# Kernel tuning notes

Measured on AMD Instinct MI355X. Metric: run time of the kernel, lower is better.

Reference implementation:

```python
import jax, jax.numpy as jnp
import numpy as np

N = 50000          # nodes
E = 800000         # edges
F_IN = 128         # in_channels
C = 64             # cell channels
NCELLS = 2
STEPS = 4
MULT = 4
N_EDGE_SLOTS = 14  # 2+3+4+5 mixed-op edges per cell
N_OPS = 8          # switch_on
NUM_CLASSES = 40
BN_EPS = 1e-5
GCNII_ALPHA = 0.1


def setup_inputs() -> dict:
    key = jax.random.key(0)
    ks = jax.random.split(key, 20)
    def w(k, shape, fan_in):
        return jax.random.normal(k, shape, dtype=jnp.float32) / np.float32(np.sqrt(fan_in))
    return {
        "x": jax.random.normal(ks[0], (N, F_IN), dtype=jnp.float32),
        "edge_index": jax.random.randint(ks[1], (2, E), 0, N, dtype=jnp.int32),
        "alphas": 0.001 * jax.random.normal(ks[2], (N_EDGE_SLOTS, N_OPS), dtype=jnp.float32),
        "stem_W": w(ks[3], (F_IN, 3 * C), F_IN),
        "pre_W": w(ks[4], (F_IN, C), F_IN),
        "pre0_W0": w(ks[5], (3 * C, C), 3 * C),
        "pre1_W0": w(ks[6], (3 * C, C), 3 * C),
        "pre0_W1": w(ks[7], (3 * C, C), 3 * C),
        "pre1_W1": w(ks[8], (MULT * C, C), MULT * C),
        "W_gcn": w(ks[9], (NCELLS, N_EDGE_SLOTS, C, C), C),
        "W_sage_self": w(ks[10], (NCELLS, N_EDGE_SLOTS, C, C), C),
        "W_sage_nei": w(ks[11], (NCELLS, N_EDGE_SLOTS, C, C), C),
        "W_gin": w(ks[12], (NCELLS, N_EDGE_SLOTS, C, C), C),
        "W_gc1": w(ks[13], (NCELLS, N_EDGE_SLOTS, C, C), C),
        "W_gc2": w(ks[14], (NCELLS, N_EDGE_SLOTS, C, C), C),
        "W_mlp": w(ks[15], (NCELLS, N_EDGE_SLOTS, C, C), C),
        "W_gcnii": w(ks[16], (NCELLS, N_EDGE_SLOTS, C, C), C),
        "cls_W": w(ks[17], (MULT * C + 1, NUM_CLASSES), MULT * C + 1),
        "cls_b": jnp.zeros((NUM_CLASSES,), dtype=jnp.float32),
    }


def reference(x, edge_index, alphas, stem_W, pre_W, pre0_W0, pre1_W0, pre0_W1, pre1_W1,
              W_gcn, W_sage_self, W_sage_nei, W_gin, W_gc1, W_gc2, W_mlp, W_gcnii,
              cls_W, cls_b):
    src, dst = edge_index[0], edge_index[1]
    deg = jax.ops.segment_sum(jnp.ones((E,), jnp.float32), dst, num_segments=N)
    deg = jnp.maximum(deg, 1.0)
    inv_deg = 1.0 / deg
    inv_sqrt = jax.lax.rsqrt(deg)
    edge_norm = (inv_sqrt[src] * inv_sqrt[dst])[:, None]  # [E,1] sym-normalized coeff

    def bn(h):  # batch norm over node axis, no affine (gamma=1, beta=0)
        m = jnp.mean(h, axis=0)
        v = jnp.var(h, axis=0)
        return (h - m) * jax.lax.rsqrt(v + BN_EPS)

    def mlp(xx, W, act):  # Linear(no bias) -> BN -> optional ReLU
        h = bn(xx @ W)
        return jnp.maximum(h, 0.0) if act else h

    relu = lambda t: jnp.maximum(t, 0.0)

    def mixed_op(h, wv, ci, ej, x0):
        # shared message-passing aggregations of h over edge_index
        msg = h[src]                                             # [E,C] gather
        s_sum = jax.ops.segment_sum(msg, dst, num_segments=N)    # sum agg
        s_mean = s_sum * inv_deg[:, None]                        # mean agg
        s_norm = jax.ops.segment_sum(msg * edge_norm, dst, num_segments=N)  # gcn agg
        out = wv[1] * h                                          # skip_connect (wv[0]: none)
        out = out + wv[2] * relu(s_norm @ W_gcn[ci, ej])
        out = out + wv[3] * (h @ W_sage_self[ci, ej] + s_mean @ W_sage_nei[ci, ej])
        out = out + wv[4] * relu((h + s_sum) @ W_gin[ci, ej])
        out = out + wv[5] * (h @ W_gc1[ci, ej] + s_sum @ W_gc2[ci, ej])
        out = out + wv[6] * relu(h @ W_mlp[ci, ej])
        out = out + wv[7] * relu(((1.0 - GCNII_ALPHA) * s_norm + GCNII_ALPHA * x0) @ W_gcnii[ci, ej])
        return out

    wmix = jax.nn.softmax(alphas, axis=-1)  # [14,8], identical across cells

    s0 = s1 = mlp(x, stem_W, act=False)     # stem: MLP([in, 3C], act=None)
    x0 = mlp(x, pre_W, act=True)            # preprocess: MLP([in, C], relu)
    pre_ws = [(pre0_W0, pre1_W0), (pre0_W1, pre1_W1)]
    for ci in range(NCELLS):
        p0, p1 = pre_ws[ci]
        a = mlp(s0, p0, act=True)
        b = mlp(s1, p1, act=True)
        states = [a, b]
        offset = 0
        for _ in range(STEPS):
            s = None
            for j, h in enumerate(states):
                o = mixed_op(h, wmix[offset + j], ci, offset + j, x0)
                s = o if s is None else s + o
            offset += len(states)
            states.append(s)
        out_cell = jnp.concatenate(states[-MULT:], axis=1)  # [N, 4C]
        s0, s1 = s1, out_cell

    pooled = jnp.mean(s1, axis=1, keepdims=True)            # AdaptiveAvgPool1d(1) over channels
    logits = jnp.concatenate([pooled, s1], axis=1) @ cls_W + cls_b
    return logits
```

## Files before the change

kernel.cpp:

```cpp
#include <hip/hip_runtime.h>
#include <stdint.h>

typedef unsigned short u16;
typedef __attribute__((ext_vector_type(8))) short bh8;
typedef __attribute__((ext_vector_type(4))) float f4;

__device__ __forceinline__ float b2f(u16 u){ union{unsigned u; float f;} x; x.u = ((unsigned)u)<<16; return x.f; }
__device__ __forceinline__ u16 f2b(float f){ union{float f; unsigned u;} x; x.f = f; return (u16)((x.u + 0x7fffu + ((x.u>>16)&1u))>>16); }
__device__ __forceinline__ bh8 ld8(const u16* p){ return *reinterpret_cast<const bh8*>(p); }

__device__ __forceinline__ int xcd_swz(int bid, int nwg){
  int q = nwg >> 3, r = nwg & 7;
  int x = bid & 7, k = bid >> 3;
  return (x < r ? x*(q+1) : r*(q+1) + (x - r)*q) + k;
}

#define NBK 512

__global__ __launch_bounds__(256) void k_hist(const int* dst, int* hist, int E){
  __shared__ int h[NBK];
  for (int i=threadIdx.x;i<NBK;i+=256) h[i]=0;
  __syncthreads();
  int stride = 256*gridDim.x;
  for (int i = blockIdx.x*256+threadIdx.x; i<E; i+=stride)
    atomicAdd(&h[dst[i]>>7], 1);
  __syncthreads();
  for (int i=threadIdx.x;i<NBK;i+=256){
    int v=h[i]; if (v) atomicAdd(&hist[i], v);
  }
}

__global__ __launch_bounds__(512) void k_scanb(const int* hist, int* bbase, int* bcursor){
  int t = threadIdx.x, lane = t&63, wv = t>>6;
  __shared__ int ws[8];
  int v = hist[t];
  int x = v;
  #pragma unroll
  for (int o=1;o<64;o<<=1){ int u=__shfl_up(x,(unsigned)o,64); if(lane>=o) x+=u; }
  if (lane==63) ws[wv]=x;
  __syncthreads();
  if (t<8){
    int s=ws[t];
    #pragma unroll
    for (int o=1;o<8;o<<=1){ int u=__shfl_up(s,(unsigned)o,8); if (t>=o) s+=u; }
    ws[t]=s;
  }
  __syncthreads();
  int base = (wv==0)?0:ws[wv-1];
  int ex = base + x - v;
  bbase[t]=ex; bcursor[t]=ex;
  if (t==511) bbase[512]=ex+v;
}

__global__ __launch_bounds__(256) void k_bucket(const int* src, const int* dst,
                                                int* bcursor, unsigned* bkt, int E, int nblk){
  __shared__ int h[NBK], base[NBK], lc[NBK];
  int per = (E + nblk - 1)/nblk;
  int e0 = blockIdx.x*per, e1 = min(E, e0+per);
  for (int i=threadIdx.x;i<NBK;i+=256){ h[i]=0; lc[i]=0; }
  __syncthreads();
  for (int e=e0+threadIdx.x; e<e1; e+=256) atomicAdd(&h[dst[e]>>7], 1);
  __syncthreads();
  for (int i=threadIdx.x;i<NBK;i+=256){
    int c=h[i]; base[i] = c ? atomicAdd(&bcursor[i], c) : 0;
  }
  __syncthreads();
  for (int e=e0+threadIdx.x; e<e1; e+=256){
    int d = dst[e];
    int b = d>>7;
    int r = atomicAdd(&lc[b], 1);
    bkt[base[b]+r] = ((unsigned)(d&127)<<25) | (unsigned)src[e];
  }
}

__global__ __launch_bounds__(128) void k_degb(const unsigned* bkt, const int* bbase,
                                              int* off, float* inv_deg, float* invs,
                                              int N, int E){
  int b = blockIdx.x, t = threadIdx.x;
  __shared__ int cnt[128];
  __shared__ int w0tot;
  cnt[t]=0;
  __syncthreads();
  int e0=bbase[b], e1=bbase[b+1];
  for (int e=e0+t; e<e1; e+=128) atomicAdd(&cnt[bkt[e]>>25], 1);
  __syncthreads();
  int v = cnt[t];
  int lane=t&63, wv=t>>6;
  int x=v;
  #pragma unroll
  for (int o=1;o<64;o<<=1){ int u=__shfl_up(x,(unsigned)o,64); if(lane>=o) x+=u; }
  if (t==63) w0tot=x;
  __syncthreads();
  int ex = x - v + (wv ? w0tot : 0);
  int node = b*128 + t;
  if (node < N){
    off[node] = e0 + ex;
    int d = (v<1)?1:v;
    float df=(float)d;
    inv_deg[node]=1.0f/df;
    invs[node]=rsqrtf(df);
  }
  if (b==0 && t==0) off[N]=E;
}

__global__ __launch_bounds__(128) void k_fillb(const unsigned* bkt, const int* bbase,
                                               const int* off, const float* invs,
                                               int2* csr, int N){
  int b = blockIdx.x, t = threadIdx.x;
  __shared__ int cur[128];
  int node = b*128 + t;
  cur[t] = (node < N) ? off[node] : 0;
  __syncthreads();
  int e0=bbase[b], e1=bbase[b+1];
  for (int e=e0+t; e<e1; e+=128){
    unsigned v = bkt[e];
    int i = (int)(v>>25);
    int s = (int)(v & 0x1FFFFFFu);
    int pos = atomicAdd(&cur[i], 1);
    csr[pos] = make_int2(s, __float_as_int(invs[s]));
  }
}

__global__ void k_softmax(const float* alphas, float* wmix){
  int t = threadIdx.x; int r = t >> 3, o = t & 7;
  if (r < 14){
    float v = alphas[r*8+o];
    float m = v;
    #pragma unroll
    for (int d=1; d<8; d<<=1) m = fmaxf(m, __shfl_xor(m, d, 8));
    float e = expf(v - m);
    float s = e;
    #pragma unroll
    for (int d=1; d<8; d<<=1) s += __shfl_xor(s, d, 8);
    wmix[r*8+o] = e / s;
  }
}

__global__ void k_f2b(const float* a, u16* b, int n){
  int i = blockIdx.x*256 + threadIdx.x;
  if (i < n) b[i] = f2b(a[i]);
}

struct PackAllArgs {
  const float* src[7];
  u16* dst[7];
  int K[7], ncol[7];
  int base[8];
};
__global__ __launch_bounds__(256) void k_packall(PackAllArgs P){
  int i = blockIdx.x*256 + threadIdx.x;
  if (i >= P.base[7]) return;
  int s = 0;
  #pragma unroll
  for (int k=1;k<7;k++) if (i >= P.base[k]) s = k;
  int e = i - P.base[s];
  if (s < 6){
    int K = P.K[s], ncol = P.ncol[s];
    int k = e / ncol, n = e - k*ncol;
    P.dst[s][(size_t)n*K + k] = f2b(P.src[s][e]);
  } else {
    int n = e >> 8, k = e & 255;
    float v = 0.f;
    if (n < 40) v = P.src[6][(size_t)(1+k)*40 + n] + P.src[6][n] * (1.f/256.f);
    P.dst[6][(size_t)n*256 + k] = f2b(v);
  }
}

struct PackArgs { const float* W[8]; const float* wmix; u16* dst; };
__global__ void k_pack_ops8(PackArgs P){
  int i = blockIdx.x*256 + threadIdx.x;
  if (i >= 28*8*4096) return;
  int slot28 = i >> 15;
  int rem = i & 32767;
  int mat = rem >> 12;
  int e = rem & 4095;
  int k = e >> 6, n = e & 63;
  const float* wm = P.wmix + (slot28 % 14)*8;
  size_t off = (size_t)slot28*4096 + e;
  float v = 0.f;
  switch(mat){
    case 0: v = wm[2]*P.W[0][off]; break;
    case 1: v = wm[3]*P.W[1][off] + wm[5]*P.W[4][off] + ((k==n) ? wm[1] : 0.f); break;
    case 2: v = wm[3]*P.W[2][off]; break;
    case 3: v = wm[4]*P.W[3][off]; break;
    case 4: v = wm[5]*P.W[5][off]; break;
    case 5: v = wm[6]*P.W[6][off]; break;
    case 6: v = 0.9f*wm[7]*P.W[7][off]; break;
    case 7: v = 0.1f*wm[7]*P.W[7][off]; break;
  }
  P.dst[(((size_t)slot28*8 + mat)<<12) + (n<<6) + (((k>>3) ^ (n&7))<<3) + (k&7)] = f2b(v);
}

template<int NT, int NKB>
__global__ __launch_bounds__(256) void k_gemm(const u16* A, const u16* Bp,
                                              u16* Tb, int Nn, float* Sp){
  const int K = NKB*32;
  const int ldT = NT*16;
  __shared__ float sred[4][NT*16][2];
  int tid = threadIdx.x, wv = tid>>6, lane = tid&63, q = lane>>4, t = lane&15;
  int row0 = blockIdx.x*128 + wv*32;
  f4 acc[2][NT];
  #pragma unroll
  for (int a=0;a<2;a++)
    #pragma unroll
    for (int b=0;b<NT;b++) acc[a][b] = (f4){0.f,0.f,0.f,0.f};
  const u16* arow0 = A + (size_t)(row0 + t)*K + q*8;
  const u16* arow1 = arow0 + (size_t)16*K;
  const u16* brow  = Bp + (size_t)t*K + q*8;
  #pragma unroll
  for (int kb = 0; kb < NKB; ++kb){
    bh8 a0 = ld8(arow0 + kb*32);
    bh8 a1 = ld8(arow1 + kb*32);
    #pragma unroll
    for (int nt=0; nt<NT; ++nt){
      bh8 bf = ld8(brow + (size_t)nt*16*K + kb*32);
      acc[0][nt] = __builtin_amdgcn_mfma_f32_16x16x32_bf16(a0, bf, acc[0][nt], 0, 0, 0);
      acc[1][nt] = __builtin_amdgcn_mfma_f32_16x16x32_bf16(a1, bf, acc[1][nt], 0, 0, 0);
    }
  }
  #pragma unroll
  for (int nt=0;nt<NT;nt++){
    float ps = 0.f, pq = 0.f;
    #pragma unroll
    for (int rt=0;rt<2;rt++)
      #pragma unroll
      for (int r=0;r<4;r++){
        int row = row0 + rt*16 + q*4 + r;
        float v = acc[rt][nt][r];
        if (row < Nn){
          Tb[(size_t)row*ldT + nt*16 + t] = f2b(v);
          ps += v; pq += v*v;
        }
      }
    ps += __shfl_xor(ps, 16, 64); pq += __shfl_xor(pq, 16, 64);
    ps += __shfl_xor(ps, 32, 64); pq += __shfl_xor(pq, 32, 64);
    if (q == 0){ sred[wv][nt*16 + t][0] = ps; sred[wv][nt*16 + t][1] = pq; }
  }
  __syncthreads();
  if (tid < NT*16){
    float s = sred[0][tid][0] + sred[1][tid][0] + sred[2][tid][0] + sred[3][tid][0];
    float qq = sred[0][tid][1] + sred[1][tid][1] + sred[2][tid][1] + sred[3][tid][1];
    float* sp = Sp + (size_t)blockIdx.x*(2*NT*16);
    sp[tid] = s;
    sp[NT*16 + tid] = qq;
  }
}

__global__ __launch_bounds__(256) void k_redstats(const float* Sp, float* S, int ncol, int nb){
  int c2 = blockIdx.x*4 + (threadIdx.x>>6);
  int lane = threadIdx.x & 63;
  if (c2 >= 2*ncol) return;
  int stride = 2*ncol;
  float s = 0.f;
  for (int b = lane; b < nb; b += 64) s += Sp[(size_t)b*stride + c2];
  #pragma unroll
  for (int m=1; m<64; m<<=1) s += __shfl_xor(s, m, 64);
  if (lane == 0){
    int c = (c2 < ncol) ? c2 : (256 + (c2 - ncol));
    S[c] = s;
  }
}

__global__ void k_norm(const u16* Tb, int ldT, int ncols, int Nn, const float* S,
                       u16* out, int rs_out, int relu, float invN){
  int i = blockIdx.x*256 + threadIdx.x;
  int nv = ncols >> 3;
  if (i >= Nn*nv) return;
  int r = i / nv, c8 = (i - r*nv)*8;
  bh8 tv = ld8(Tb + (size_t)r*ldT + c8);
  bh8 ov;
  #pragma unroll
  for (int u=0; u<8; ++u){
    int c = c8 + u;
    float m = S[c]*invN;
    float var = S[256+c]*invN - m*m;
    float xv = (b2f((u16)tv[u]) - m) * rsqrtf(var + 1e-5f);
    if (relu) xv = fmaxf(xv, 0.f);
    ov[u] = (short)f2b(xv);
  }
  *reinterpret_cast<bh8*>(out + (size_t)r*rs_out + c8) = ov;
}

__global__ void k_norm2(const u16* Tb, int Nn, const float* S,
                        u16* o1, u16* o2, float invN){
  int i = blockIdx.x*256 + threadIdx.x;
  if (i >= Nn*32) return;
  int r = i >> 5, c8 = (i & 31) << 3;
  bh8 tv = ld8(Tb + (size_t)r*256 + c8);
  bh8 ov;
  int relu = (c8 >= 192);
  #pragma unroll
  for (int u=0; u<8; ++u){
    int c = c8 + u;
    float m = S[c]*invN;
    float var = S[256+c]*invN - m*m;
    float xv = (b2f((u16)tv[u]) - m) * rsqrtf(var + 1e-5f);
    if (relu) xv = fmaxf(xv, 0.f);
    ov[u] = (short)f2b(xv);
  }
  if (c8 < 192)
    *reinterpret_cast<bh8*>(o1 + (size_t)r*192 + c8) = ov;
  else
    *reinterpret_cast<bh8*>(o2 + (size_t)r*64 + (c8 - 192)) = ov;
}

#define ACC8(vv, ww) { \
    float c0=__uint_as_float((vv).x<<16), c1=__uint_as_float((vv).x&0xffff0000u); \
    float c2=__uint_as_float((vv).y<<16), c3=__uint_as_float((vv).y&0xffff0000u); \
    float c4=__uint_as_float((vv).z<<16), c5=__uint_as_float((vv).z&0xffff0000u); \
    float c6=__uint_as_float((vv).w<<16), c7=__uint_as_float((vv).w&0xffff0000u); \
    s0+=c0; s1+=c1; s2+=c2; s3+=c3; s4+=c4; s5+=c5; s6+=c6; s7+=c7; \
    n0+=c0*(ww); n1+=c1*(ww); n2+=c2*(ww); n3+=c3*(ww); \
    n4+=c4*(ww); n5+=c5*(ww); n6+=c6*(ww); n7+=c7*(ww); }

template<int SHIFT>
__global__ __launch_bounds__(256) void k_aggv(const u16* h, const int* off, const int2* csr,
                                              const float* inv_sqrt, u16* out_sum, u16* out_norm, int Nn){
  int blk = xcd_swz(blockIdx.x, gridDim.x);
  int g = blk*8 + (threadIdx.x >> 5);
  if (g >= Nn) return;
  int l32 = threadIdx.x & 31;
  int sub = l32 >> 3;
  int cb = (l32 & 7) << 3;
  const u16* hp = h + cb;
  float s0=0,s1=0,s2=0,s3=0,s4=0,s5=0,s6=0,s7=0;
  float n0=0,n1=0,n2=0,n3=0,n4=0,n5=0,n6=0,n7=0;
  int e0 = off[g], e1 = off[g+1];
  int e = e0 + sub;
  for (; e + 12 < e1; e += 16){
    int2 cA = csr[e];
    int2 cB = csr[e+4];
    int2 cC = csr[e+8];
    int2 cD = csr[e+12];
    uint4 vA = *reinterpret_cast<const uint4*>(hp + (((unsigned)cA.x) << SHIFT));
    uint4 vB = *reinterpret_cast<const uint4*>(hp + (((unsigned)cB.x) << SHIFT));
    uint4 vC = *reinterpret_cast<const uint4*>(hp + (((unsigned)cC.x) << SHIFT));
    uint4 vD = *reinterpret_cast<const uint4*>(hp + (((unsigned)cD.x) << SHIFT));
    float wA = __int_as_float(cA.y), wB = __int_as_float(cB.y);
    float wC = __int_as_float(cC.y), wD = __int_as_float(cD.y);
    ACC8(vA, wA)
    ACC8(vB, wB)
    ACC8(vC, wC)
    ACC8(vD, wD)
  }
  for (; e < e1; e += 4){
    int2 cA = csr[e];
    uint4 vA = *reinterpret_cast<const uint4*>(hp + (((unsigned)cA.x) << SHIFT));
    float wA = __int_as_float(cA.y);
    ACC8(vA, wA)
  }
  #pragma unroll
  for (int m = 8; m <= 16; m <<= 1){
    s0 += __shfl_xor(s0,m,64); s1 += __shfl_xor(s1,m,64);
    s2 += __shfl_xor(s2,m,64); s3 += __shfl_xor(s3,m,64);
    s4 += __shfl_xor(s4,m,64); s5 += __shfl_xor(s5,m,64);
    s6 += __shfl_xor(s6,m,64); s7 += __shfl_xor(s7,m,64);
    n0 += __shfl_xor(n0,m,64); n1 += __shfl_xor(n1,m,64);
    n2 += __shfl_xor(n2,m,64); n3 += __shfl_xor(n3,m,64);
    n4 += __shfl_xor(n4,m,64); n5 += __shfl_xor(n5,m,64);
    n6 += __shfl_xor(n6,m,64); n7 += __shfl_xor(n7,m,64);
  }
  if (sub == 0){
    float ig = inv_sqrt[g];
    uint4 o;
    o.x = (uint)f2b(s0) | ((uint)f2b(s1) << 16);
    o.y = (uint)f2b(s2) | ((uint)f2b(s3) << 16);
    o.z = (uint)f2b(s4) | ((uint)f2b(s5) << 16);
    o.w = (uint)f2b(s6) | ((uint)f2b(s7) << 16);
    *reinterpret_cast<uint4*>(out_sum + (size_t)g*64 + cb) = o;
    o.x = (uint)f2b(n0*ig) | ((uint)f2b(n1*ig) << 16);
    o.y = (uint)f2b(n2*ig) | ((uint)f2b(n3*ig) << 16);
    o.z = (uint)f2b(n4*ig) | ((uint)f2b(n5*ig) << 16);
    o.w = (uint)f2b(n6*ig) | ((uint)f2b(n7*ig) << 16);
    *reinterpret_cast<uint4*>(out_norm + (size_t)g*64 + cb) = o;
  }
}

#define ACC8AB(va, vb, ww) { \
    float a0=__uint_as_float((va).x<<16), a1=__uint_as_float((va).x&0xffff0000u); \
    float a2=__uint_as_float((va).y<<16), a3=__uint_as_float((va).y&0xffff0000u); \
    float a4=__uint_as_float((va).z<<16), a5=__uint_as_float((va).z&0xffff0000u); \
    float a6=__uint_as_float((va).w<<16), a7=__uint_as_float((va).w&0xffff0000u); \
    float b0=__uint_as_float((vb).x<<16), b1=__uint_as_float((vb).x&0xffff0000u); \
    float b2=__uint_as_float((vb).y<<16), b3=__uint_as_float((vb).y&0xffff0000u); \
    float b4=__uint_as_float((vb).z<<16), b5=__uint_as_float((vb).z&0xffff0000u); \
    float b6=__uint_as_float((vb).w<<16), b7=__uint_as_float((vb).w&0xffff0000u); \
    sa0+=a0; sa1+=a1; sa2+=a2; sa3+=a3; sa4+=a4; sa5+=a5; sa6+=a6; sa7+=a7; \
    na0+=a0*(ww); na1+=a1*(ww); na2+=a2*(ww); na3+=a3*(ww); \
    na4+=a4*(ww); na5+=a5*(ww); na6+=a6*(ww); na7+=a7*(ww); \
    sb0+=b0; sb1+=b1; sb2+=b2; sb3+=b3; sb4+=b4; sb5+=b5; sb6+=b6; sb7+=b7; \
    nb0+=b0*(ww); nb1+=b1*(ww); nb2+=b2*(ww); nb3+=b3*(ww); \
    nb4+=b4*(ww); nb5+=b5*(ww); nb6+=b6*(ww); nb7+=b7*(ww); }

__global__ __launch_bounds__(256) void k_agg2v(const u16* ab, const int* off, const int2* csr,
                                               const float* inv_sqrt,
                                               u16* os0, u16* on0, u16* os1, u16* on1, int Nn){
  int blk = xcd_swz(blockIdx.x, gridDim.x);
  int g = blk*8 + (threadIdx.x >> 5);
  if (g >= Nn) return;
  int l32 = threadIdx.x & 31;
  int sub = l32 >> 3;
  int cb = (l32 & 7) << 3;
  const u16* hp = ab + cb;
  float sa0=0,sa1=0,sa2=0,sa3=0,sa4=0,sa5=0,sa6=0,sa7=0;
  float na0=0,na1=0,na2=0,na3=0,na4=0,na5=0,na6=0,na7=0;
  float sb0=0,sb1=0,sb2=0,sb3=0,sb4=0,sb5=0,sb6=0,sb7=0;
  float nb0=0,nb1=0,nb2=0,nb3=0,nb4=0,nb5=0,nb6=0,nb7=0;
  int e0 = off[g], e1 = off[g+1];
  int e = e0 + sub;
  for (; e + 4 < e1; e += 8){
    int2 cA = csr[e];
    int2 cB = csr[e+4];
    const u16* rpA = hp + (((unsigned)cA.x) << 7);
    const u16* rpB = hp + (((unsigned)cB.x) << 7);
    uint4 vaA = *reinterpret_cast<const uint4*>(rpA);
    uint4 vbA = *reinterpret_cast<const uint4*>(rpA + 64);
    uint4 vaB = *reinterpret_cast<const uint4*>(rpB);
    uint4 vbB = *reinterpret_cast<const uint4*>(rpB + 64);
    float wA = __int_as_float(cA.y), wB = __int_as_float(cB.y);
    ACC8AB(vaA, vbA, wA)
    ACC8AB(vaB, vbB, wB)
  }
  if (e < e1){
    int2 cA = csr[e];
    const u16* rpA = hp + (((unsigned)cA.x) << 7);
    uint4 vaA = *reinterpret_cast<const uint4*>(rpA);
    uint4 vbA = *reinterpret_cast<const uint4*>(rpA + 64);
    float wA = __int_as_float(cA.y);
    ACC8AB(vaA, vbA, wA)
  }
  #pragma unroll
  for (int m = 8; m <= 16; m <<= 1){
    sa0 += __shfl_xor(sa0,m,64); sa1 += __shfl_xor(sa1,m,64);
    sa2 += __shfl_xor(sa2,m,64); sa3 += __shfl_xor(sa3,m,64);
    sa4 += __shfl_xor(sa4,m,64); sa5 += __shfl_xor(sa5,m,64);
    sa6 += __shfl_xor(sa6,m,64); sa7 += __shfl_xor(sa7,m,64);
    na0 += __shfl_xor(na0,m,64); na1 += __shfl_xor(na1,m,64);
    na2 += __shfl_xor(na2,m,64); na3 += __shfl_xor(na3,m,64);
    na4 += __shfl_xor(na4,m,64); na5 += __shfl_xor(na5,m,64);
    na6 += __shfl_xor(na6,m,64); na7 += __shfl_xor(na7,m,64);
    sb0 += __shfl_xor(sb0,m,64); sb1 += __shfl_xor(sb1,m,64);
    sb2 += __shfl_xor(sb2,m,64); sb3 += __shfl_xor(sb3,m,64);
    sb4 += __shfl_xor(sb4,m,64); sb5 += __shfl_xor(sb5,m,64);
    sb6 += __shfl_xor(sb6,m,64); sb7 += __shfl_xor(sb7,m,64);
    nb0 += __shfl_xor(nb0,m,64); nb1 += __shfl_xor(nb1,m,64);
    nb2 += __shfl_xor(nb2,m,64); nb3 += __shfl_xor(nb3,m,64);
    nb4 += __shfl_xor(nb4,m,64); nb5 += __shfl_xor(nb5,m,64);
    nb6 += __shfl_xor(nb6,m,64); nb7 += __shfl_xor(nb7,m,64);
  }
  if (sub == 0){
    float ig = inv_sqrt[g];
    uint4 o;
    o.x = (uint)f2b(sa0) | ((uint)f2b(sa1) << 16);
    o.y = (uint)f2b(sa2) | ((uint)f2b(sa3) << 16);
    o.z = (uint)f2b(sa4) | ((uint)f2b(sa5) << 16);
    o.w = (uint)f2b(sa6) | ((uint)f2b(sa7) << 16);
    *reinterpret_cast<uint4*>(os0 + (size_t)g*64 + cb) = o;
    o.x = (uint)f2b(na0*ig) | ((uint)f2b(na1*ig) << 16);
    o.y = (uint)f2b(na2*ig) | ((uint)f2b(na3*ig) << 16);
    o.z = (uint)f2b(na4*ig) | ((uint)f2b(na5*ig) << 16);
    o.w = (uint)f2b(na6*ig) | ((uint)f2b(na7*ig) << 16);
    *reinterpret_cast<uint4*>(on0 + (size_t)g*64 + cb) = o;
    o.x = (uint)f2b(sb0) | ((uint)f2b(sb1) << 16);
    o.y = (uint)f2b(sb2) | ((uint)f2b(sb3) << 16);
    o.z = (uint)f2b(sb4) | ((uint)f2b(sb5) << 16);
    o.w = (uint)f2b(sb6) | ((uint)f2b(sb7) << 16);
    *reinterpret_cast<uint4*>(os1 + (size_t)g*64 + cb) = o;
    o.x = (uint)f2b(nb0*ig) | ((uint)f2b(nb1*ig) << 16);
    o.y = (uint)f2b(nb2*ig) | ((uint)f2b(nb3*ig) << 16);
    o.z = (uint)f2b(nb4*ig) | ((uint)f2b(nb5*ig) << 16);
    o.w = (uint)f2b(nb6*ig) | ((uint)f2b(nb7*ig) << 16);
    *reinterpret_cast<uint4*>(on1 + (size_t)g*64 + cb) = o;
  }
}

struct StepArgs {
  const u16* h[5]; const u16* asum[5]; const u16* anorm[5];
  int rs[5]; int slot[5]; int J;
  const u16* wpk; const float* inv_deg; const u16* x0;
  u16* out; int rs_out; int Nn;
};

__device__ __forceinline__ void mm8(const bh8 (&af)[2], const u16* wlds, int mat,
                                    int t, int q, f4 (&acc)[4]){
  #pragma unroll
  for (int kb=0;kb<2;kb++)
    #pragma unroll
    for (int nt=0;nt<4;nt++){
      bh8 bf = ld8(wlds + (mat<<12) + ((nt*16+t)<<6) + ((((kb<<2)|q) ^ (t&7))<<3));
      acc[nt] = __builtin_amdgcn_mfma_f32_16x16x32_bf16(af[kb], bf, acc[nt], 0, 0, 0);
    }
}

__global__ __launch_bounds__(512)
void k_step(StepArgs A){
  __shared__ __align__(16) u16 wlds[8*4096];
  int tid = threadIdx.x, wv = tid>>6, lane = tid&63, q = lane>>4, t = lane&15;
  int blk = xcd_swz(blockIdx.x, gridDim.x);
  int row0 = blk*128 + wv*16;
  int rA = row0 + t;
  int q8 = q*8;
  f4 idg = *reinterpret_cast<const f4*>(A.inv_deg + row0 + q*4);
  const u16* xp = A.x0 + (size_t)rA*64;
  bh8 fx[2];
  fx[0]=ld8(xp+q8); fx[1]=ld8(xp+32+q8);

  f4 oacc[4];
  #pragma unroll
  for (int b=0;b<4;b++) oacc[b] = (f4){0.f,0.f,0.f,0.f};

  uint4* wdst = reinterpret_cast<uint4*>(wlds);
  for (int j = 0; j < A.J; ++j){
    if (j) __syncthreads();
    const uint4* wsrc = reinterpret_cast<const uint4*>(A.wpk) + ((size_t)A.slot[j] << 12);
    #pragma unroll
    for (int i = 0; i < 8; ++i) wdst[tid + i*512] = wsrc[tid + i*512];

    const u16* h = A.h[j]; int rs = A.rs[j];
    const u16* hp = h + (size_t)rA*rs;
    const u16* sp = A.asum[j] + (size_t)rA*64;
    const u16* np = A.anorm[j] + (size_t)rA*64;
    bh8 fh[2], fs[2], fn[2];
    fh[0]=ld8(hp+q8); fh[1]=ld8(hp+32+q8);
    fs[0]=ld8(sp+q8); fs[1]=ld8(sp+32+q8);
    fn[0]=ld8(np+q8); fn[1]=ld8(np+32+q8);

    __syncthreads();

    mm8(fh, wlds, 1, t, q, oacc);
    mm8(fs, wlds, 4, t, q, oacc);
    f4 p[4];
    #pragma unroll
    for (int b=0;b<4;b++) p[b] = (f4){0.f,0.f,0.f,0.f};
    mm8(fh, wlds, 5, t, q, p);
    #pragma unroll
    for (int nt=0;nt<4;nt++)
      #pragma unroll
      for (int r=0;r<4;r++) oacc[nt][r] += fmaxf(p[nt][r], 0.f);
    #pragma unroll
    for (int b=0;b<4;b++) p[b] = (f4){0.f,0.f,0.f,0.f};
    mm8(fh, wlds, 3, t, q, p);
    mm8(fs, wlds, 3, t, q, p);
    #pragma unroll
    for (int nt=0;nt<4;nt++)
      #pragma unroll
      for (int r=0;r<4;r++) oacc[nt][r] += fmaxf(p[nt][r], 0.f);
    #pragma unroll
    for (int b=0;b<4;b++) p[b] = (f4){0.f,0.f,0.f,0.f};
    mm8(fn, wlds, 0, t, q, p);
    #pragma unroll
    for (int nt=0;nt<4;nt++)
      #pragma unroll
      for (int r=0;r<4;r++) oacc[nt][r] += fmaxf(p[nt][r], 0.f);
    #pragma unroll
    for (int b=0;b<4;b++) p[b] = (f4){0.f,0.f,0.f,0.f};
    mm8(fn, wlds, 6, t, q, p);
    mm8(fx, wlds, 7, t, q, p);
    #pragma unroll
    for (int nt=0;nt<4;nt++)
      #pragma unroll
      for (int r=0;r<4;r++) oacc[nt][r] += fmaxf(p[nt][r], 0.f);
    #pragma unroll
    for (int b=0;b<4;b++) p[b] = (f4){0.f,0.f,0.f,0.f};
    mm8(fs, wlds, 2, t, q, p);
    #pragma unroll
    for (int nt=0;nt<4;nt++)
      #pragma unroll
      for (int r=0;r<4;r++) oacc[nt][r] += idg[r]*p[nt][r];
  }

  #pragma unroll
  for (int nt=0;nt<4;nt++)
    #pragma unroll
    for (int r=0;r<4;r++){
      int rr = row0 + q*4 + r;
      if (rr < A.Nn) A.out[(size_t)rr*A.rs_out + nt*16 + t] = f2b(oacc[nt][r]);
    }
}

__global__ __launch_bounds__(256) void k_cls_mm(const u16* A, const u16* Bp,
                                                const float* bvec, float* out, int Nn){
  int tid = threadIdx.x, wv = tid>>6, lane = tid&63, q = lane>>4, t = lane&15;
  int row0 = blockIdx.x*128 + wv*32;
  f4 acc[2][3];
  #pragma unroll
  for (int a=0;a<2;a++)
    #pragma unroll
    for (int b=0;b<3;b++) acc[a][b] = (f4){0.f,0.f,0.f,0.f};
  const u16* arow0 = A + (size_t)(row0 + t)*256 + q*8;
  const u16* arow1 = arow0 + (size_t)16*256;
  const u16* brow  = Bp + (size_t)t*256 + q*8;
  #pragma unroll
  for (int kb = 0; kb < 8; ++kb){
    bh8 a0 = ld8(arow0 + kb*32);
    bh8 a1 = ld8(arow1 + kb*32);
    #pragma unroll
    for (int nt=0; nt<3; ++nt){
      bh8 bf = ld8(brow + (size_t)nt*16*256 + kb*32);
      acc[0][nt] = __builtin_amdgcn_mfma_f32_16x16x32_bf16(a0, bf, acc[0][nt], 0, 0, 0);
      acc[1][nt] = __builtin_amdgcn_mfma_f32_16x16x32_bf16(a1, bf, acc[1][nt], 0, 0, 0);
    }
  }
  #pragma unroll
  for (int rt=0;rt<2;rt++)
    #pragma unroll
    for (int nt=0;nt<3;nt++){
      int col = nt*16 + t;
      #pragma unroll
      for (int r=0;r<4;r++){
        int row = row0 + rt*16 + q*4 + r;
        if (row < Nn && col < 40) out[(size_t)row*40 + col] = acc[rt][nt][r] + bvec[col];
      }
    }
}

extern "C" void kernel_launch(void* const* d_in, const int* in_sizes, int n_in,
                              void* d_out, int out_size, void* d_ws, size_t ws_size,
                              hipStream_t stream){
  (void)n_in; (void)out_size; (void)ws_size;
  const float* x      = (const float*)d_in[0];
  const int*   ei     = (const int*)d_in[1];
  const float* alphas = (const float*)d_in[2];
  const float* stem_W = (const float*)d_in[3];
  const float* pre_W  = (const float*)d_in[4];
  const float* p00    = (const float*)d_in[5];
  const float* p10    = (const float*)d_in[6];
  const float* p01    = (const float*)d_in[7];
  const float* p11    = (const float*)d_in[8];
  const float* clsW = (const float*)d_in[17];
  const float* clsb = (const float*)d_in[18];

  int N = in_sizes[0] / 128;
  int E = in_sizes[1] / 2;
  const int* esrc = ei;
  const int* edst = ei + E;

  char* p = (char*)d_ws;
  auto carve = [&](size_t bytes) -> char* {
    char* r = p; p += (bytes + 255) & ~(size_t)255; return r;
  };
  int*   hist    = (int*)carve((size_t)NBK*4);
  int*   bbase   = (int*)carve((size_t)(NBK+1)*4);
  int*   bcursor = (int*)carve((size_t)NBK*4);
  unsigned* bkt  = (unsigned*)carve((size_t)E*4);
  int*   off     = (int*)carve((size_t)(N+1)*4);
  int2*  csr     = (int2*)carve((size_t)E*8);
  float* inv_deg = (float*)carve((size_t)N*4);
  float* invs    = (float*)carve((size_t)N*4);
  float* wmix    = (float*)carve(14*8*4);
  float* stats   = (float*)carve(512*4);
  float* Sp      = (float*)carve((size_t)512*512*4);
  u16* xb      = (u16*)carve((size_t)N*128*2);
  u16* spk     = (u16*)carve((size_t)256*128*2);
  u16* p00_pk  = (u16*)carve((size_t)64*192*2);
  u16* p10_pk  = (u16*)carve((size_t)64*192*2);
  u16* p01_pk  = (u16*)carve((size_t)64*192*2);
  u16* p11_pk  = (u16*)carve((size_t)64*256*2);
  u16* cls_pk  = (u16*)carve((size_t)48*256*2);
  u16* ops_pk  = (u16*)carve((size_t)28*8*4096*2);
  u16* T       = (u16*)carve((size_t)N*256*2);
  u16* stem_o  = (u16*)carve((size_t)N*192*2);
  u16* x0b     = (u16*)carve((size_t)N*64*2);
  u16* ab      = (u16*)carve((size_t)N*128*2);
  u16* oc0     = (u16*)carve((size_t)N*256*2);
  u16* oc1     = (u16*)carve((size_t)N*256*2);
  u16* agg     = (u16*)carve((size_t)5*2*N*64*2);
  carve(262144);

  auto aggS = [&](int j){ return agg + (size_t)j*2*N*64; };
  auto aggN = [&](int j){ return agg + (size_t)j*2*N*64 + (size_t)N*64; };

  int NB = (N + 127)/128;
  int gg = (N + 127)/128;
  int gstep = (N + 127)/128;
  int ag = (N + 7)/8;
  float invN = 1.0f/(float)N;

  hipMemsetAsync(hist, 0, (size_t)NBK*4, stream);
  k_hist<<<256,256,0,stream>>>(edst, hist, E);
  k_scanb<<<1,512,0,stream>>>(hist, bbase, bcursor);
  k_bucket<<<256,256,0,stream>>>(esrc, edst, bcursor, bkt, E, 256);
  k_degb<<<NB,128,0,stream>>>(bkt, bbase, off, inv_deg, invs, N, E);
  k_fillb<<<NB,128,0,stream>>>(bkt, bbase, off, invs, csr, N);

  k_softmax<<<1,128,0,stream>>>(alphas, wmix);
  k_f2b<<<(N*128+255)/256,256,0,stream>>>(x, xb, N*128);

  {
    PackAllArgs PA;
    PA.src[0]=stem_W; PA.dst[0]=spk;          PA.K[0]=128; PA.ncol[0]=192;
    PA.src[1]=pre_W;  PA.dst[1]=spk+192*128;  PA.K[1]=128; PA.ncol[1]=64;
    PA.src[2]=p00;    PA.dst[2]=p00_pk;       PA.K[2]=192; PA.ncol[2]=64;
    PA.src[3]=p10;    PA.dst[3]=p10_pk;       PA.K[3]=192; PA.ncol[3]=64;
    PA.src[4]=p01;    PA.dst[4]=p01_pk;       PA.K[4]=192; PA.ncol[4]=64;
    PA.src[5]=p11;    PA.dst[5]=p11_pk;       PA.K[5]=256; PA.ncol[5]=64;
    PA.src[6]=clsW;   PA.dst[6]=cls_pk;
    PA.K[6]=0; PA.ncol[6]=0;
    int b = 0;
    PA.base[0]=0;
    int sizes[7] = {128*192, 128*64, 192*64, 192*64, 192*64, 256*64, 48*256};
    for (int s=0;s<7;s++){ b += sizes[s]; PA.base[s+1]=b; }
    k_packall<<<(b+255)/256,256,0,stream>>>(PA);
  }
  {
    PackArgs PA;
    for (int i = 0; i < 8; ++i) PA.W[i] = (const float*)d_in[9+i];
    PA.wmix = wmix; PA.dst = ops_pk;
    k_pack_ops8<<<(28*8*4096+255)/256,256,0,stream>>>(PA);
  }

  auto mlp = [&](const u16* A, int K, const u16* Bp, int ncol, u16* outb, int rs_out, int relu){
    if (K == 192)
      hipLaunchKernelGGL(HIP_KERNEL_NAME(k_gemm<4,6>), dim3(gg), dim3(256), 0, stream, A, Bp, T, N, Sp);
    else
      hipLaunchKernelGGL(HIP_KERNEL_NAME(k_gemm<4,8>), dim3(gg), dim3(256), 0, stream, A, Bp, T, N, Sp);
    k_redstats<<<(2*ncol+3)/4,256,0,stream>>>(Sp, stats, ncol, gg);
    k_norm<<<((N*(ncol>>3))+255)/256,256,0,stream>>>(T, ncol, ncol, N, stats, outb, rs_out, relu, invN);
  };

  hipLaunchKernelGGL(HIP_KERNEL_NAME(k_gemm<16,4>), dim3(gg), dim3(256), 0, stream, xb, spk, T, N, Sp);
  k_redstats<<<(512+3)/4,256,0,stream>>>(Sp, stats, 256, gg);
  k_norm2<<<(N*32+255)/256,256,0,stream>>>(T, N, stats, stem_o, x0b, invN);

  u16* ocs[2] = {oc0, oc1};
  const int slotbase[4] = {0, 2, 5, 9};
  for (int ci = 0; ci < 2; ++ci){
    const u16* s1in = (ci == 0) ? stem_o : oc0;
    int Kb   = (ci == 0) ? 192 : 256;
    const u16* pa = (ci == 0) ? p00_pk : p01_pk;
    const u16* pb = (ci == 0) ? p10_pk : p11_pk;
    mlp(stem_o, 192, pa, 64, ab, 128, 1);
    mlp(s1in, Kb, pb, 64, ab + 64, 128, 1);

    u16* oc = ocs[ci];
    const u16* wpk_cell = ops_pk + (size_t)ci*14*8*4096;

    k_agg2v<<<ag,256,0,stream>>>(ab, off, csr, invs,
                                 aggS(0), aggN(0), aggS(1), aggN(1), N);

    const u16* st[5] = { ab, ab + 64, oc + 0, oc + 64, oc + 128 };
    const int strs[5] = {128, 128, 256, 256, 256};
    for (int step = 0; step < 4; ++step){
      StepArgs SA{};
      int J = step + 2;
      for (int j = 0; j < J; ++j){
        SA.h[j] = st[j]; SA.rs[j] = strs[j];
        SA.asum[j] = aggS(j); SA.anorm[j] = aggN(j);
        SA.slot[j] = slotbase[step] + j;
      }
      SA.J = J; SA.wpk = wpk_cell; SA.inv_deg = inv_deg; SA.x0 = x0b;
      SA.out = oc + (size_t)step*64; SA.rs_out = 256; SA.Nn = N;
      k_step<<<gstep,512,0,stream>>>(SA);
      if (step < 3)
        hipLaunchKernelGGL(HIP_KERNEL_NAME(k_aggv<8>), dim3(ag), dim3(256), 0, stream,
                           oc + (size_t)step*64, off, csr, invs, aggS(step+2), aggN(step+2), N);
    }
  }

  k_cls_mm<<<gg,256,0,stream>>>(oc1, cls_pk, clsb, (float*)d_out, N);
}
```

Measured before the change: 770.9 us.

## Split step-kernel weight staging into halves to overlap loads with MFMA

The packed weights are permuted so the eight matrices of each slot fall into two halves in the order the step kernel uses them. The step kernel now stages each half into its own LDS buffer. It computes on the first half while the second half loads, then prefetches the next slot's first half while computing on the second. This aims to hide global-to-LDS weight copy latency behind matrix work, at the cost of more complex barrier placement. Total LDS use is unchanged.

```diff
diff --git a/kernel.cpp b/kernel.cpp
--- a/kernel.cpp
+++ b/kernel.cpp
@@ -188,7 +188,8 @@
     case 6: v = 0.9f*wm[7]*P.W[7][off]; break;
     case 7: v = 0.1f*wm[7]*P.W[7][off]; break;
   }
-  P.dst[(((size_t)slot28*8 + mat)<<12) + (n<<6) + (((k>>3) ^ (n&7))<<3) + (k&7)] = f2b(v);
+  const int perm[8] = {4,0,7,3,1,2,5,6};
+  P.dst[(((size_t)slot28*8 + perm[mat])<<12) + (n<<6) + (((k>>3) ^ (n&7))<<3) + (k&7)] = f2b(v);
 }
 
 template<int NT, int NKB>
@@ -481,20 +482,20 @@
   u16* out; int rs_out; int Nn;
 };
 
-__device__ __forceinline__ void mm8(const bh8 (&af)[2], const u16* wlds, int mat,
+__device__ __forceinline__ void mm8(const bh8 (&af)[2], const u16* wb, int mat,
                                     int t, int q, f4 (&acc)[4]){
   #pragma unroll
   for (int kb=0;kb<2;kb++)
     #pragma unroll
     for (int nt=0;nt<4;nt++){
-      bh8 bf = ld8(wlds + (mat<<12) + ((nt*16+t)<<6) + ((((kb<<2)|q) ^ (t&7))<<3));
+      bh8 bf = ld8(wb + (mat<<12) + ((nt*16+t)<<6) + ((((kb<<2)|q) ^ (t&7))<<3));
       acc[nt] = __builtin_amdgcn_mfma_f32_16x16x32_bf16(af[kb], bf, acc[nt], 0, 0, 0);
     }
 }
 
 __global__ __launch_bounds__(512)
 void k_step(StepArgs A){
-  __shared__ __align__(16) u16 wlds[8*4096];
+  __shared__ __align__(16) u16 wlds[2][4*4096];
   int tid = threadIdx.x, wv = tid>>6, lane = tid&63, q = lane>>4, t = lane&15;
   int blk = xcd_swz(blockIdx.x, gridDim.x);
   int row0 = blk*128 + wv*16;
@@ -509,12 +510,18 @@
   #pragma unroll
   for (int b=0;b<4;b++) oacc[b] = (f4){0.f,0.f,0.f,0.f};
 
-  uint4* wdst = reinterpret_cast<uint4*>(wlds);
+  auto stageH = [&](int slot, int half, int buf){
+    const uint4* ws = reinterpret_cast<const uint4*>(A.wpk) + ((size_t)slot << 12) + (half<<11);
+    uint4* wd = reinterpret_cast<uint4*>(&wlds[buf][0]);
+    #pragma unroll
+    for (int i=0;i<4;i++) wd[tid + i*512] = ws[tid + i*512];
+  };
+
+  stageH(A.slot[0], 0, 0);
+  __syncthreads();
+
   for (int j = 0; j < A.J; ++j){
-    if (j) __syncthreads();
-    const uint4* wsrc = reinterpret_cast<const uint4*>(A.wpk) + ((size_t)A.slot[j] << 12);
-    #pragma unroll
-    for (int i = 0; i < 8; ++i) wdst[tid + i*512] = wsrc[tid + i*512];
+    stageH(A.slot[j], 1, 1);
 
     const u16* h = A.h[j]; int rs = A.rs[j];
     const u16* hp = h + (size_t)rA*rs;
@@ -525,48 +532,55 @@
     fs[0]=ld8(sp+q8); fs[1]=ld8(sp+32+q8);
     fn[0]=ld8(np+q8); fn[1]=ld8(np+32+q8);
 
-    __syncthreads();
-
-    mm8(fh, wlds, 1, t, q, oacc);
-    mm8(fs, wlds, 4, t, q, oacc);
+    const u16* b0 = &wlds[0][0];
+    mm8(fh, b0, 0, t, q, oacc);
+    mm8(fs, b0, 1, t, q, oacc);
     f4 p[4];
     #pragma unroll
     for (int b=0;b<4;b++) p[b] = (f4){0.f,0.f,0.f,0.f};
-    mm8(fh, wlds, 5, t, q, p);
+    mm8(fh, b0, 2, t, q, p);
     #pragma unroll
     for (int nt=0;nt<4;nt++)
       #pragma unroll
       for (int r=0;r<4;r++) oacc[nt][r] += fmaxf(p[nt][r], 0.f);
     #pragma unroll
     for (int b=0;b<4;b++) p[b] = (f4){0.f,0.f,0.f,0.f};
-    mm8(fh, wlds, 3, t, q, p);
-    mm8(fs, wlds, 3, t, q, p);
+    mm8(fh, b0, 3, t, q, p);
+    mm8(fs, b0, 3, t, q, p);
     #pragma unroll
     for (int nt=0;nt<4;nt++)
       #pragma unroll
       for (int r=0;r<4;r++) oacc[nt][r] += fmaxf(p[nt][r], 0.f);
+
+    __syncthreads();
+
+    if (j+1 < A.J) stageH(A.slot[j+1], 0, 0);
+
+    const u16* b1 = &wlds[1][0];
     #pragma unroll
     for (int b=0;b<4;b++) p[b] = (f4){0.f,0.f,0.f,0.f};
-    mm8(fn, wlds, 0, t, q, p);
+    mm8(fn, b1, 0, t, q, p);
     #pragma unroll
     for (int nt=0;nt<4;nt++)
       #pragma unroll
       for (int r=0;r<4;r++) oacc[nt][r] += fmaxf(p[nt][r], 0.f);
     #pragma unroll
     for (int b=0;b<4;b++) p[b] = (f4){0.f,0.f,0.f,0.f};
-    mm8(fn, wlds, 6, t, q, p);
-    mm8(fx, wlds, 7, t, q, p);
+    mm8(fn, b1, 1, t, q, p);
+    mm8(fx, b1, 2, t, q, p);
     #pragma unroll
     for (int nt=0;nt<4;nt++)
       #pragma unroll
       for (int r=0;r<4;r++) oacc[nt][r] += fmaxf(p[nt][r], 0.f);
     #pragma unroll
     for (int b=0;b<4;b++) p[b] = (f4){0.f,0.f,0.f,0.f};
-    mm8(fs, wlds, 2, t, q, p);
+    mm8(fs, b1, 3, t, q, p);
     #pragma unroll
     for (int nt=0;nt<4;nt++)
       #pragma unroll
       for (int r=0;r<4;r++) oacc[nt][r] += idg[r]*p[nt][r];
+
+    if (j+1 < A.J) __syncthreads();
   }
 
   #pragma unroll
```

After: 780.1 us. Within noise of the previous version (+1.2%).
